# Optimization experiments

Measured on AMD Instinct MI355X. Metric: run time of the kernel, lower is better.

## Reference

```python
import jax, jax.numpy as jnp
import numpy as np

THRESHOLD = 1.0
SLOPE = 25.0  # snntorch surrogate.fast_sigmoid default slope
BETA = 0.9

@jax.custom_vjp
def spike_fn(x):
    # Heaviside forward, fast-sigmoid surrogate backward: g / (slope*|x| + 1)^2
    return (x > 0).astype(x.dtype)

def _spike_fwd(x):
    return spike_fn(x), x

def _spike_bwd(x, g):
    return (g / (SLOPE * jnp.abs(x) + 1.0) ** 2,)

spike_fn.defvjp(_spike_fwd, _spike_bwd)


def setup_inputs() -> dict:
    key = jax.random.key(0)
    k_x, k_w1, k_b1, k_w2, k_b2 = jax.random.split(key, 5)
    B, T, F, H, O = 128, 256, 2500, 128, 2
    x = jax.random.normal(k_x, (B, T, F), dtype=jnp.float32)
    # PyTorch Linear init: U(-1/sqrt(fan_in), 1/sqrt(fan_in))
    s1 = 1.0 / np.sqrt(F)
    s2 = 1.0 / np.sqrt(H)
    W1 = jax.random.uniform(k_w1, (H, F), jnp.float32, -s1, s1)
    b1 = jax.random.uniform(k_b1, (H,), jnp.float32, -s1, s1)
    W2 = jax.random.uniform(k_w2, (O, H), jnp.float32, -s2, s2)
    b2 = jax.random.uniform(k_b2, (O,), jnp.float32, -s2, s2)
    return {"x": x, "W1": W1, "b1": b1, "W2": W2, "b2": b2}


def reference(x, W1, b1, W2, b2):
    # Module transposes to [time, batch, feat] when shape[0] < shape[1]
    if x.ndim == 3 and x.shape[0] < x.shape[1]:
        x = jnp.swapaxes(x, 0, 1)  # [T, B, F]
    T, B = x.shape[0], x.shape[1]
    H, O = W1.shape[0], W2.shape[0]

    def lif(mem, cur):
        # snntorch Leaky, reset_mechanism='subtract'; reset spike is detached
        rst = jax.lax.stop_gradient(spike_fn(mem - THRESHOLD))
        mem = BETA * mem + cur - rst * THRESHOLD
        spk = spike_fn(mem - THRESHOLD)
        return spk, mem

    def step(carry, xt):
        mem1, mem2 = carry
        cur1 = xt @ W1.T + b1            # [B, H]
        spk1, mem1 = lif(mem1, cur1)
        cur2 = spk1 @ W2.T + b2          # [B, O]
        spk2, mem2 = lif(mem2, cur2)
        return (mem1, mem2), (spk2, mem2)

    mem1_0 = jnp.zeros((B, H), x.dtype)
    mem2_0 = jnp.zeros((B, O), x.dtype)
    _, (spk_rec, mem_rec) = jax.lax.scan(step, (mem1_0, mem2_0), x)
    return spk_rec, mem_rec  # each [T, B, O]
```

## Files before the change

### kernel.cpp

```cpp
#include <hip/hip_runtime.h>

#define T_STEPS 256
#define B_SZ    128
#define F_SZ    2500
#define F4      625
#define F_P     2528
#define NSTEP   79
#define H_SZ    128
#define O_SZ    2
#define FLAG_WINDOW 8e-5
#define CHUNK   12

typedef unsigned short U16;
typedef short  s16x8 __attribute__((ext_vector_type(8)));
typedef U16    u16x8 __attribute__((ext_vector_type(8)));
typedef float  f32x4 __attribute__((ext_vector_type(4)));

__device__ __forceinline__ U16 bf16_rne(float f) {
    unsigned u = __float_as_uint(f);
    u += 0x7FFFu + ((u >> 16) & 1u);
    return (U16)(u >> 16);
}

__global__ __launch_bounds__(256) void k_split(const float* __restrict__ W1,
                                               U16* __restrict__ W1h,
                                               U16* __restrict__ W1l,
                                               int* __restrict__ nh) {
    const int h = blockIdx.x;
    if (h == 0 && threadIdx.x < B_SZ) nh[threadIdx.x] = 0;
    for (int k = threadIdx.x; k < F_P; k += 256) {
        const float w = (k < F_SZ) ? W1[(size_t)h * F_SZ + k] : 0.f;
        const U16 hi = bf16_rne(w);
        const float hf = __uint_as_float((unsigned)hi << 16);
        W1h[(size_t)h * F_P + k] = hi;
        W1l[(size_t)h * F_P + k] = bf16_rne(w - hf);
    }
}

__global__ __launch_bounds__(256, 2) void k_gemm(const float* __restrict__ x,
                                                 const U16* __restrict__ W1h,
                                                 const U16* __restrict__ W1l,
                                                 float* __restrict__ cur1) {
    __shared__ __align__(16) U16 Alds[2][128 * 64];
    __shared__ __align__(16) U16 Blds[2][64 * 64];

    const int tid = threadIdx.x;
    const int t   = blockIdx.x >> 1;
    const int h0  = (blockIdx.x & 1) << 6;

    const int ra   = tid >> 1;
    const int kq   = (tid & 1) << 4;
    const int aswz = ra & 7;
    const int au0  = (tid & 1) << 1;
    const float* xp = x + ((size_t)ra * T_STEPS + t) * F_SZ + kq;

    const int rb  = tid >> 2;
    const int ub0 = (tid & 3) << 1;
    const U16* bsrc[2];
    #pragma unroll
    for (int c = 0; c < 2; ++c) {
        const int lu = (ub0 + c) ^ (rb & 7);
        const U16* base = (lu < 4) ? (W1h + lu * 8) : (W1l + (lu - 4) * 8);
        bsrc[c] = base + (size_t)(h0 + rb) * F_P;
    }

    const int wid = tid >> 6, lane = tid & 63;
    const int wm0 = (wid >> 1) << 6;
    const int wn0 = (wid & 1) << 5;
    const int lr = lane & 15, lg = lane >> 4;

    f32x4 acc[4][2];
    #pragma unroll
    for (int i = 0; i < 4; ++i)
        #pragma unroll
        for (int j = 0; j < 2; ++j) {
            acc[i][j][0] = 0.f; acc[i][j][1] = 0.f; acc[i][j][2] = 0.f; acc[i][j][3] = 0.f;
        }

    float4 xr[4];
    u16x8  br[2];

    auto loadX = [&](int kk) {
        #pragma unroll
        for (int c = 0; c < 4; ++c) {
            const int k = kk + kq + c * 4;
            xr[c] = (k < F_SZ) ? *(const float4*)(xp + kk + c * 4)
                               : make_float4(0.f, 0.f, 0.f, 0.f);
        }
    };
    auto loadB = [&](int kk) {
        #pragma unroll
        for (int c = 0; c < 2; ++c) br[c] = *(const u16x8*)(bsrc[c] + kk);
    };
    auto stage = [&](int bb) {
        U16* Ab = Alds[bb];
        U16* Bb = Blds[bb];
        u16x8 vh[2], vl[2];
        #pragma unroll
        for (int p = 0; p < 2; ++p) {
            const float* f0 = (const float*)&xr[p * 2];
            const float* f1 = (const float*)&xr[p * 2 + 1];
            #pragma unroll
            for (int j = 0; j < 4; ++j) {
                const float v0 = f0[j], v1 = f1[j];
                const U16 hv0 = bf16_rne(v0);
                const U16 hv1 = bf16_rne(v1);
                vh[p][j]     = hv0;
                vh[p][4 + j] = hv1;
                vl[p][j]     = bf16_rne(v0 - __uint_as_float((unsigned)hv0 << 16));
                vl[p][4 + j] = bf16_rne(v1 - __uint_as_float((unsigned)hv1 << 16));
            }
        }
        #pragma unroll
        for (int p = 0; p < 2; ++p) {
            *(u16x8*)(Ab + ra * 64 + (((au0 + p) ^ aswz) << 3))       = vh[p];
            *(u16x8*)(Ab + ra * 64 + (((au0 + p + 4) ^ aswz) << 3))   = vl[p];
        }
        #pragma unroll
        for (int c = 0; c < 2; ++c)
            *(u16x8*)(Bb + rb * 64 + ((ub0 + c) << 3)) = br[c];
    };

    loadX(0);
    loadB(0);
    stage(0);

    int bb = 0;
    #pragma unroll 1
    for (int s = 0; s < NSTEP; ++s) {
        __syncthreads();
        const bool more = (s + 1 < NSTEP);
        if (more) { loadX((s + 1) * 32); loadB((s + 1) * 32); }

        const U16* Ab = Alds[bb];
        const U16* Bb = Blds[bb];
        s16x8 ah[4], al[4], bh[2], blo[2];
        #pragma unroll
        for (int fi = 0; fi < 4; ++fi) {
            const int m = wm0 + fi * 16 + lr;
            const int msw = m & 7;
            ah[fi] = *(const s16x8*)(Ab + m * 64 + ((lg ^ msw) << 3));
            al[fi] = *(const s16x8*)(Ab + m * 64 + (((lg + 4) ^ msw) << 3));
        }
        #pragma unroll
        for (int fj = 0; fj < 2; ++fj) {
            const int n = wn0 + fj * 16 + lr;
            const int nsw = n & 7;
            bh[fj]  = *(const s16x8*)(Bb + n * 64 + ((lg ^ nsw) << 3));
            blo[fj] = *(const s16x8*)(Bb + n * 64 + (((lg + 4) ^ nsw) << 3));
        }
        #pragma unroll
        for (int fi = 0; fi < 4; ++fi)
            #pragma unroll
            for (int fj = 0; fj < 2; ++fj) {
                acc[fi][fj] = __builtin_amdgcn_mfma_f32_16x16x32_bf16(ah[fi], bh[fj],  acc[fi][fj], 0, 0, 0);
                acc[fi][fj] = __builtin_amdgcn_mfma_f32_16x16x32_bf16(ah[fi], blo[fj], acc[fi][fj], 0, 0, 0);
                acc[fi][fj] = __builtin_amdgcn_mfma_f32_16x16x32_bf16(al[fi], bh[fj],  acc[fi][fj], 0, 0, 0);
                acc[fi][fj] = __builtin_amdgcn_mfma_f32_16x16x32_bf16(al[fi], blo[fj], acc[fi][fj], 0, 0, 0);
            }

        if (more) stage(bb ^ 1);
        bb ^= 1;
    }

    #pragma unroll
    for (int fi = 0; fi < 4; ++fi)
        #pragma unroll
        for (int fj = 0; fj < 2; ++fj) {
            const int hcol = h0 + wn0 + fj * 16 + lr;
            #pragma unroll
            for (int r = 0; r < 4; ++r) {
                const int brow = wm0 + fi * 16 + lg * 4 + r;
                cur1[((size_t)t * B_SZ + brow) * H_SZ + hcol] = acc[fi][fj][r];
            }
        }
}

__global__ __launch_bounds__(256) void k_lif1(const float* __restrict__ cur1,
                                              const float* __restrict__ b1,
                                              unsigned long long* __restrict__ spk_bits,
                                              int* __restrict__ nh,
                                              int* __restrict__ hlist) {
    const int idx = blockIdx.x * 256 + threadIdx.x;
    const int b = idx >> 7, h = idx & 127;
    const double b1v = (double)b1[h];
    double mem = 0.0;
    bool flagged = false;
    #pragma unroll 4
    for (int t = 0; t < T_STEPS; ++t) {
        const double cur = (double)cur1[(size_t)t * 16384 + idx] + b1v;
        const double rst = (mem > 1.0) ? 1.0 : 0.0;
        mem = fma(0.9, mem, cur) - rst;
        const bool spk = (mem > 1.0);
        const unsigned long long m = __ballot(spk);
        if ((threadIdx.x & 63) == 0)
            spk_bits[((size_t)t * B_SZ + b) * 2 + ((h >> 6) & 1)] = m;
        if (!flagged && fabs(mem - 1.0) < FLAG_WINDOW) {
            flagged = true;
            int s = atomicAdd(&nh[b], 1);
            hlist[b * 128 + s] = h;
        }
    }
}

__global__ __launch_bounds__(256) void k_cur2(const unsigned long long* __restrict__ bits,
                                              const float* __restrict__ W2,
                                              const float* __restrict__ b2,
                                              double* __restrict__ cur2) {
    __shared__ float w2s[256];
    w2s[threadIdx.x] = W2[threadIdx.x];
    __syncthreads();
    const int pair = blockIdx.x * 256 + threadIdx.x;
    unsigned long long m0 = bits[(size_t)pair * 2];
    unsigned long long m1 = bits[(size_t)pair * 2 + 1];
    double v0 = (double)b2[0], v1 = (double)b2[1];
    while (m0) {
        const int i = __ffsll((long long)m0) - 1; m0 &= m0 - 1;
        v0 += (double)w2s[i]; v1 += (double)w2s[128 + i];
    }
    while (m1) {
        const int i = __ffsll((long long)m1) - 1; m1 &= m1 - 1;
        v0 += (double)w2s[64 + i]; v1 += (double)w2s[192 + i];
    }
    cur2[(size_t)pair * 2]     = v0;
    cur2[(size_t)pair * 2 + 1] = v1;
}

__global__ __launch_bounds__(256) void k_fixA(const float* __restrict__ x,
                                              const float* __restrict__ W1,
                                              const int* __restrict__ nh,
                                              const int* __restrict__ hlist,
                                              double* __restrict__ cur_fix) {
    const int b   = blockIdx.x >> 4;
    const int tch = blockIdx.x & 15;
    const int n   = nh[b];
    if (n == 0) return;

    __shared__ float w1s[CHUNK * F_SZ];
    const int tid  = threadIdx.x;
    const int wv   = tid >> 6;
    const int lane = tid & 63;

    for (int c0 = 0; c0 < n; c0 += CHUNK) {
        const int nc = (n - c0 < CHUNK) ? (n - c0) : CHUNK;
        __syncthreads();
        for (int r = 0; r < nc; ++r) {
            const int h = hlist[b * 128 + c0 + r];
            const float4* src = (const float4*)W1 + (size_t)h * F4;
            float4* dst = (float4*)(w1s + r * F_SZ);
            for (int c = tid; c < F4; c += 256) dst[c] = src[c];
        }
        __syncthreads();

        #pragma unroll 1
        for (int tt = 0; tt < 4; ++tt) {
            const int t = tch * 16 + wv * 4 + tt;
            float4 xv[10];
            const float4* xb = (const float4*)x + ((size_t)b * T_STEPS + t) * F4;
            #pragma unroll
            for (int j = 0; j < 10; ++j) {
                const int c = lane + 64 * j;
                xv[j] = (c < F4) ? xb[c] : make_float4(0.f, 0.f, 0.f, 0.f);
            }
            for (int s = 0; s < nc; ++s) {
                const float* wr = w1s + s * F_SZ;
                double p = 0.0;
                #pragma unroll
                for (int j = 0; j < 10; ++j) {
                    const int c = lane + 64 * j;
                    if (c < F4) {
                        const float4 w4 = *(const float4*)(wr + c * 4);
                        p = fma((double)xv[j].x, (double)w4.x, p);
                        p = fma((double)xv[j].y, (double)w4.y, p);
                        p = fma((double)xv[j].z, (double)w4.z, p);
                        p = fma((double)xv[j].w, (double)w4.w, p);
                    }
                }
                #pragma unroll
                for (int off = 32; off >= 1; off >>= 1) p += __shfl_down(p, off);
                if (lane == 0)
                    cur_fix[((size_t)b * 128 + c0 + s) * T_STEPS + t] = p;
            }
        }
    }
}

__global__ __launch_bounds__(128) void k_fixB(const float* __restrict__ cur1,
                                              const double* __restrict__ cur_fix,
                                              const float* __restrict__ b1,
                                              const float* __restrict__ W2,
                                              const int* __restrict__ nh,
                                              const int* __restrict__ hlist,
                                              double* __restrict__ cur2) {
    const int b = blockIdx.x;
    const int s = threadIdx.x;
    if (s >= nh[b]) return;
    const int h = hlist[b * 128 + s];
    const double b1v = (double)b1[h];
    const double w0 = (double)W2[h], w1 = (double)W2[128 + h];
    double ma = 0.0, me = 0.0;
    for (int t = 0; t < T_STEPS; ++t) {
        const double ca = (double)cur1[((size_t)t * B_SZ + b) * H_SZ + h] + b1v;
        const double ce = cur_fix[((size_t)b * 128 + s) * T_STEPS + t] + b1v;
        const double ra = (ma > 1.0) ? 1.0 : 0.0;
        const double re = (me > 1.0) ? 1.0 : 0.0;
        ma = fma(0.9, ma, ca) - ra;
        me = fma(0.9, me, ce) - re;
        const bool sa = (ma > 1.0), se = (me > 1.0);
        if (sa != se) {
            const double d = se ? 1.0 : -1.0;
            atomicAdd(&cur2[((size_t)t * B_SZ + b) * 2 + 0], d * w0);
            atomicAdd(&cur2[((size_t)t * B_SZ + b) * 2 + 1], d * w1);
        }
    }
}

__global__ __launch_bounds__(256) void k_lif2(const double* __restrict__ cur2,
                                              float* __restrict__ out) {
    const int tid = threadIdx.x;
    double mem = 0.0;
    float* spk_out = out;
    float* mem_out = out + T_STEPS * B_SZ * O_SZ;
    #pragma unroll 8
    for (int t = 0; t < T_STEPS; ++t) {
        const double cur = cur2[t * 256 + tid];
        const double rst = (mem > 1.0) ? 1.0 : 0.0;
        mem = fma(0.9, mem, cur) - rst;
        spk_out[t * 256 + tid] = (mem > 1.0) ? 1.0f : 0.0f;
        mem_out[t * 256 + tid] = (float)mem;
    }
}

extern "C" void kernel_launch(void* const* d_in, const int* in_sizes, int n_in,
                              void* d_out, int out_size, void* d_ws, size_t ws_size,
                              hipStream_t stream) {
    const float* x  = (const float*)d_in[0];
    const float* W1 = (const float*)d_in[1];
    const float* b1 = (const float*)d_in[2];
    const float* W2 = (const float*)d_in[3];
    const float* b2 = (const float*)d_in[4];
    float* out = (float*)d_out;

    char* ws = (char*)d_ws;
    float*  cur1    = (float*)ws;
    U16*    W1h     = (U16*)(ws + 16777216);
    U16*    W1l     = (U16*)(ws + 17424384);
    double* cur2    = (double*)(ws + 18071552);
    double* cur_fix = (double*)(ws + 18595840);
    unsigned long long* spk_bits = (unsigned long long*)(ws + 18595840);
    int*    nh      = (int*)(ws + 52150272);
    int*    hlist   = (int*)(ws + 52150784);

    k_split<<<128, 256, 0, stream>>>(W1, W1h, W1l, nh);
    k_gemm<<<512, 256, 0, stream>>>(x, W1h, W1l, cur1);
    k_lif1<<<64, 256, 0, stream>>>(cur1, b1, spk_bits, nh, hlist);
    k_cur2<<<128, 256, 0, stream>>>(spk_bits, W2, b2, cur2);
    k_fixA<<<2048, 256, 0, stream>>>(x, W1, nh, hlist, cur_fix);
    k_fixB<<<128, 128, 0, stream>>>(cur1, cur_fix, b1, W2, nh, hlist, cur2);
    k_lif2<<<1, 256, 0, stream>>>(cur2, out);
}
```

Measured before the change: 789.5 us.

## Split-K GEMM with pre-swizzled W1 tiles loaded directly into LDS

The W1 hi/lo bf16 split kernel now writes a pre-swizzled per-k-tile image, so the GEMM can copy B tiles straight from global memory into LDS with global_load_lds instead of going through registers. The GEMM is split along K into two halves, doubling the block count to 1024, and blocks are remapped across XCDs. Occupancy is raised to 3 blocks per CU. The two partial sums go to separate buffers and are added in k_lif1, which writes the merged value back; this costs extra global traffic and reorders the float summation.

```diff
diff --git a/kernel.cpp b/kernel.cpp
--- a/kernel.cpp
+++ b/kernel.cpp
@@ -1,10 +1,10 @@
 #include <hip/hip_runtime.h>
+#include <hip/hip_bf16.h>
 
 #define T_STEPS 256
 #define B_SZ    128
 #define F_SZ    2500
 #define F4      625
-#define F_P     2528
 #define NSTEP   79
 #define H_SZ    128
 #define O_SZ    2
@@ -16,55 +16,69 @@
 typedef U16    u16x8 __attribute__((ext_vector_type(8)));
 typedef float  f32x4 __attribute__((ext_vector_type(4)));
 
-__device__ __forceinline__ U16 bf16_rne(float f) {
-    unsigned u = __float_as_uint(f);
-    u += 0x7FFFu + ((u >> 16) & 1u);
-    return (U16)(u >> 16);
+__device__ __forceinline__ U16 bf16c(float f) {
+    union { __hip_bfloat16 h; U16 u; } cv;
+    cv.h = __float2bfloat16(f);
+    return cv.u;
+}
+__device__ __forceinline__ float bf2f(U16 u) { return __uint_as_float((unsigned)u << 16); }
+
+__device__ __forceinline__ void gld16(const void* g, void* l) {
+    __builtin_amdgcn_global_load_lds((const __attribute__((address_space(1))) void*)g,
+                                     (__attribute__((address_space(3))) void*)l, 16, 0, 0);
 }
 
 __global__ __launch_bounds__(256) void k_split(const float* __restrict__ W1,
-                                               U16* __restrict__ W1h,
-                                               U16* __restrict__ W1l,
+                                               U16* __restrict__ Wimg,
                                                int* __restrict__ nh) {
-    const int h = blockIdx.x;
-    if (h == 0 && threadIdx.x < B_SZ) nh[threadIdx.x] = 0;
-    for (int k = threadIdx.x; k < F_P; k += 256) {
-        const float w = (k < F_SZ) ? W1[(size_t)h * F_SZ + k] : 0.f;
-        const U16 hi = bf16_rne(w);
-        const float hf = __uint_as_float((unsigned)hi << 16);
-        W1h[(size_t)h * F_P + k] = hi;
-        W1l[(size_t)h * F_P + k] = bf16_rne(w - hf);
-    }
-}
-
-__global__ __launch_bounds__(256, 2) void k_gemm(const float* __restrict__ x,
-                                                 const U16* __restrict__ W1h,
-                                                 const U16* __restrict__ W1l,
+    const int bid = blockIdx.x;
+    const int p = bid / NSTEP, kt = bid - p * NSTEP;
+    if (bid == 0 && threadIdx.x < B_SZ) nh[threadIdx.x] = 0;
+    U16* img = Wimg + ((size_t)bid << 12);
+    #pragma unroll
+    for (int c = 0; c < 2; ++c) {
+        const int v  = c * 256 + threadIdx.x;
+        const int r  = v >> 3, u = v & 7;
+        const int lu = u ^ (r & 7);
+        const int kb = kt * 32 + (lu & 3) * 8;
+        const int h  = p * 64 + r;
+        u16x8 o;
+        #pragma unroll
+        for (int e = 0; e < 8; ++e) {
+            const int k = kb + e;
+            const float w = (k < F_SZ) ? W1[(size_t)h * F_SZ + k] : 0.f;
+            const U16 hi = bf16c(w);
+            o[e] = (lu < 4) ? hi : bf16c(w - bf2f(hi));
+        }
+        *(u16x8*)(img + (size_t)v * 8) = o;
+    }
+}
+
+__global__ __launch_bounds__(256, 3) void k_gemm(const float* __restrict__ x,
+                                                 const U16* __restrict__ Wimg,
                                                  float* __restrict__ cur1) {
     __shared__ __align__(16) U16 Alds[2][128 * 64];
     __shared__ __align__(16) U16 Blds[2][64 * 64];
 
+    const int g   = blockIdx.x;
+    const int wg  = (g & 7) * 128 + (g >> 3);
+    const int t   = wg >> 2;
+    const int p   = (wg >> 1) & 1;
+    const int kh  = wg & 1;
+    const int kt0 = kh ? 40 : 0;
+    const int nst = kh ? 39 : 40;
+
     const int tid = threadIdx.x;
-    const int t   = blockIdx.x >> 1;
-    const int h0  = (blockIdx.x & 1) << 6;
 
     const int ra   = tid >> 1;
     const int kq   = (tid & 1) << 4;
+    const int au0  = (tid & 1) << 1;
     const int aswz = ra & 7;
-    const int au0  = (tid & 1) << 1;
-    const float* xp = x + ((size_t)ra * T_STEPS + t) * F_SZ + kq;
-
-    const int rb  = tid >> 2;
-    const int ub0 = (tid & 3) << 1;
-    const U16* bsrc[2];
-    #pragma unroll
-    for (int c = 0; c < 2; ++c) {
-        const int lu = (ub0 + c) ^ (rb & 7);
-        const U16* base = (lu < 4) ? (W1h + lu * 8) : (W1l + (lu - 4) * 8);
-        bsrc[c] = base + (size_t)(h0 + rb) * F_P;
-    }
-
-    const int wid = tid >> 6, lane = tid & 63;
+    const float* xrow = x + ((size_t)ra * T_STEPS + t) * F_SZ;
+
+    const char* wbase = (const char*)Wimg + ((size_t)p * NSTEP << 13);
+
+    const int lane = tid & 63, wid = tid >> 6;
     const int wm0 = (wid >> 1) << 6;
     const int wn0 = (wid & 1) << 5;
     const int lr = lane & 15, lg = lane >> 4;
@@ -78,63 +92,56 @@
         }
 
     float4 xr[4];
-    u16x8  br[2];
-
-    auto loadX = [&](int kk) {
+
+    auto loadX = [&](int kt) {
+        const int kk = kt * 32;
         #pragma unroll
         for (int c = 0; c < 4; ++c) {
             const int k = kk + kq + c * 4;
-            xr[c] = (k < F_SZ) ? *(const float4*)(xp + kk + c * 4)
-                               : make_float4(0.f, 0.f, 0.f, 0.f);
+            xr[c] = (k < F_SZ) ? *(const float4*)(xrow + k) : make_float4(0.f, 0.f, 0.f, 0.f);
         }
     };
-    auto loadB = [&](int kk) {
-        #pragma unroll
-        for (int c = 0; c < 2; ++c) br[c] = *(const u16x8*)(bsrc[c] + kk);
+    auto loadB = [&](int kt, int bb) {
+        const char* src = wbase + ((size_t)kt << 13) + (tid << 4);
+        char* dst = (char*)Blds[bb] + (tid << 4);
+        gld16(src, dst);
+        gld16(src + 4096, dst + 4096);
     };
-    auto stage = [&](int bb) {
+    auto stageA = [&](int bb) {
         U16* Ab = Alds[bb];
-        U16* Bb = Blds[bb];
-        u16x8 vh[2], vl[2];
-        #pragma unroll
-        for (int p = 0; p < 2; ++p) {
-            const float* f0 = (const float*)&xr[p * 2];
-            const float* f1 = (const float*)&xr[p * 2 + 1];
+        #pragma unroll
+        for (int pq = 0; pq < 2; ++pq) {
+            const float* f0 = (const float*)&xr[pq * 2];
+            const float* f1 = (const float*)&xr[pq * 2 + 1];
+            u16x8 vh, vl;
             #pragma unroll
             for (int j = 0; j < 4; ++j) {
-                const float v0 = f0[j], v1 = f1[j];
-                const U16 hv0 = bf16_rne(v0);
-                const U16 hv1 = bf16_rne(v1);
-                vh[p][j]     = hv0;
-                vh[p][4 + j] = hv1;
-                vl[p][j]     = bf16_rne(v0 - __uint_as_float((unsigned)hv0 << 16));
-                vl[p][4 + j] = bf16_rne(v1 - __uint_as_float((unsigned)hv1 << 16));
-            }
-        }
-        #pragma unroll
-        for (int p = 0; p < 2; ++p) {
-            *(u16x8*)(Ab + ra * 64 + (((au0 + p) ^ aswz) << 3))       = vh[p];
-            *(u16x8*)(Ab + ra * 64 + (((au0 + p + 4) ^ aswz) << 3))   = vl[p];
-        }
-        #pragma unroll
-        for (int c = 0; c < 2; ++c)
-            *(u16x8*)(Bb + rb * 64 + ((ub0 + c) << 3)) = br[c];
+                const U16 h0v = bf16c(f0[j]);
+                const U16 h1v = bf16c(f1[j]);
+                vh[j]     = h0v;
+                vh[4 + j] = h1v;
+                vl[j]     = bf16c(f0[j] - bf2f(h0v));
+                vl[4 + j] = bf16c(f1[j] - bf2f(h1v));
+            }
+            *(u16x8*)(Ab + ra * 64 + (((au0 + pq) ^ aswz) << 3))     = vh;
+            *(u16x8*)(Ab + ra * 64 + (((au0 + pq + 4) ^ aswz) << 3)) = vl;
+        }
     };
 
-    loadX(0);
-    loadB(0);
-    stage(0);
+    loadB(kt0, 0);
+    loadX(kt0);
+    stageA(0);
 
     int bb = 0;
     #pragma unroll 1
-    for (int s = 0; s < NSTEP; ++s) {
+    for (int s = 0; s < nst; ++s) {
         __syncthreads();
-        const bool more = (s + 1 < NSTEP);
-        if (more) { loadX((s + 1) * 32); loadB((s + 1) * 32); }
+        const bool more = (s + 1 < nst);
+        if (more) { loadB(kt0 + s + 1, bb ^ 1); loadX(kt0 + s + 1); }
 
         const U16* Ab = Alds[bb];
         const U16* Bb = Blds[bb];
-        s16x8 ah[4], al[4], bh[2], blo[2];
+        s16x8 ah[4], al[4], bh[2], bl[2];
         #pragma unroll
         for (int fi = 0; fi < 4; ++fi) {
             const int m = wm0 + fi * 16 + lr;
@@ -146,37 +153,38 @@
         for (int fj = 0; fj < 2; ++fj) {
             const int n = wn0 + fj * 16 + lr;
             const int nsw = n & 7;
-            bh[fj]  = *(const s16x8*)(Bb + n * 64 + ((lg ^ nsw) << 3));
-            blo[fj] = *(const s16x8*)(Bb + n * 64 + (((lg + 4) ^ nsw) << 3));
+            bh[fj] = *(const s16x8*)(Bb + n * 64 + ((lg ^ nsw) << 3));
+            bl[fj] = *(const s16x8*)(Bb + n * 64 + (((lg + 4) ^ nsw) << 3));
         }
         #pragma unroll
         for (int fi = 0; fi < 4; ++fi)
             #pragma unroll
             for (int fj = 0; fj < 2; ++fj) {
-                acc[fi][fj] = __builtin_amdgcn_mfma_f32_16x16x32_bf16(ah[fi], bh[fj],  acc[fi][fj], 0, 0, 0);
-                acc[fi][fj] = __builtin_amdgcn_mfma_f32_16x16x32_bf16(ah[fi], blo[fj], acc[fi][fj], 0, 0, 0);
-                acc[fi][fj] = __builtin_amdgcn_mfma_f32_16x16x32_bf16(al[fi], bh[fj],  acc[fi][fj], 0, 0, 0);
-                acc[fi][fj] = __builtin_amdgcn_mfma_f32_16x16x32_bf16(al[fi], blo[fj], acc[fi][fj], 0, 0, 0);
-            }
-
-        if (more) stage(bb ^ 1);
+                acc[fi][fj] = __builtin_amdgcn_mfma_f32_16x16x32_bf16(ah[fi], bh[fj], acc[fi][fj], 0, 0, 0);
+                acc[fi][fj] = __builtin_amdgcn_mfma_f32_16x16x32_bf16(ah[fi], bl[fj], acc[fi][fj], 0, 0, 0);
+                acc[fi][fj] = __builtin_amdgcn_mfma_f32_16x16x32_bf16(al[fi], bh[fj], acc[fi][fj], 0, 0, 0);
+                acc[fi][fj] = __builtin_amdgcn_mfma_f32_16x16x32_bf16(al[fi], bl[fj], acc[fi][fj], 0, 0, 0);
+            }
+
+        if (more) stageA(bb ^ 1);
         bb ^= 1;
     }
 
+    float* outp = cur1 + (size_t)kh * 4194304;
     #pragma unroll
     for (int fi = 0; fi < 4; ++fi)
         #pragma unroll
         for (int fj = 0; fj < 2; ++fj) {
-            const int hcol = h0 + wn0 + fj * 16 + lr;
+            const int hcol = (p << 6) + wn0 + fj * 16 + lr;
             #pragma unroll
             for (int r = 0; r < 4; ++r) {
                 const int brow = wm0 + fi * 16 + lg * 4 + r;
-                cur1[((size_t)t * B_SZ + brow) * H_SZ + hcol] = acc[fi][fj][r];
-            }
-        }
-}
-
-__global__ __launch_bounds__(256) void k_lif1(const float* __restrict__ cur1,
+                outp[((size_t)t * B_SZ + brow) * H_SZ + hcol] = acc[fi][fj][r];
+            }
+        }
+}
+
+__global__ __launch_bounds__(256) void k_lif1(float* __restrict__ cur1,
                                               const float* __restrict__ b1,
                                               unsigned long long* __restrict__ spk_bits,
                                               int* __restrict__ nh,
@@ -188,7 +196,11 @@
     bool flagged = false;
     #pragma unroll 4
     for (int t = 0; t < T_STEPS; ++t) {
-        const double cur = (double)cur1[(size_t)t * 16384 + idx] + b1v;
+        const float p0 = cur1[(size_t)t * 16384 + idx];
+        const float p1 = cur1[4194304 + (size_t)t * 16384 + idx];
+        const float mrg = p0 + p1;
+        cur1[(size_t)t * 16384 + idx] = mrg;
+        const double cur = (double)mrg + b1v;
         const double rst = (mem > 1.0) ? 1.0 : 0.0;
         mem = fma(0.9, mem, cur) - rst;
         const bool spk = (mem > 1.0);
@@ -343,16 +355,15 @@
 
     char* ws = (char*)d_ws;
     float*  cur1    = (float*)ws;
-    U16*    W1h     = (U16*)(ws + 16777216);
-    U16*    W1l     = (U16*)(ws + 17424384);
-    double* cur2    = (double*)(ws + 18071552);
-    double* cur_fix = (double*)(ws + 18595840);
-    unsigned long long* spk_bits = (unsigned long long*)(ws + 18595840);
+    double* cur_fix = (double*)(ws + 16777216);
+    U16*    Wimg    = (U16*)(ws + 50331648);
+    unsigned long long* spk_bits = (unsigned long long*)(ws + 50331648);
+    double* cur2    = (double*)(ws + 51625984);
     int*    nh      = (int*)(ws + 52150272);
     int*    hlist   = (int*)(ws + 52150784);
 
-    k_split<<<128, 256, 0, stream>>>(W1, W1h, W1l, nh);
-    k_gemm<<<512, 256, 0, stream>>>(x, W1h, W1l, cur1);
+    k_split<<<158, 256, 0, stream>>>(W1, Wimg, nh);
+    k_gemm<<<1024, 256, 0, stream>>>(x, Wimg, cur1);
     k_lif1<<<64, 256, 0, stream>>>(cur1, b1, spk_bits, nh, hlist);
     k_cur2<<<128, 256, 0, stream>>>(spk_bits, W2, b2, cur2);
     k_fixA<<<2048, 256, 0, stream>>>(x, W1, nh, hlist, cur_fix);
```

Result: no change. 778.9 us (-1.3%).
